# Kernel optimization log

Measured on AMD Instinct MI355X. Metric: run time of the kernel, lower is better.

## Reference

```python
import jax, jax.numpy as jnp
import numpy as np

HEADS = 16
HEAD_DIM = 64
DIM = 1024
WH, WW = 32, 32
ROPE_DIM = 32  # = HEAD_DIM // 2
ROPE_BASE = 10000
EPS = 1e-6


def _rope_cache():
    # theta: [ROPE_DIM//2]
    theta = 1.0 / (ROPE_BASE ** (jnp.arange(0, ROPE_DIM, 2, dtype=jnp.float32)[: ROPE_DIM // 2] / ROPE_DIM))
    n = WH * WW
    idx = jnp.arange(n, dtype=jnp.float32)
    x_pos = idx % WW
    y_pos = idx // WW
    freqs = jnp.concatenate([x_pos[:, None] * theta[None, :], y_pos[:, None] * theta[None, :]], axis=-1)  # [n, ROPE_DIM]
    return jnp.cos(freqs), jnp.sin(freqs)


def _apply_rope(x, cos, sin):
    # x: [b, h, n, HEAD_DIM] -> pairs [b, h, n, ROPE_DIM, 2]
    xf = x.astype(jnp.float32).reshape(*x.shape[:-1], -1, 2)
    x0, x1 = xf[..., 0], xf[..., 1]
    c = cos[None, None, :, :]
    s = sin[None, None, :, :]
    out = jnp.stack([x0 * c - x1 * s, x1 * c + x0 * s], axis=-1)
    return out.reshape(*x.shape).astype(x.dtype)


def setup_inputs() -> dict:
    key = jax.random.key(0)
    ks = jax.random.split(key, 5)
    b, n = 16, WH * WW
    inner = HEADS * HEAD_DIM
    return {
        "x": jax.random.normal(ks[0], (b, n, DIM), dtype=jnp.float32),
        "t": jax.random.normal(ks[1], (b, DIM), dtype=jnp.float32),
        "norm_w": jnp.ones((DIM,), dtype=jnp.float32),
        "mod_w": jax.random.normal(ks[2], (2 * DIM, DIM), dtype=jnp.float32) * (DIM ** -0.5),
        "qkv_w": jax.random.normal(ks[3], (3 * inner, DIM), dtype=jnp.float32) * (DIM ** -0.5),
        "wo_w": jax.random.normal(ks[4], (DIM, inner), dtype=jnp.float32) * (inner ** -0.5),
    }


def reference(x, t, norm_w, mod_w, qkv_w, wo_w):
    b, n, dim = x.shape
    scale = HEAD_DIM ** -0.5

    # Modulated RMSNorm
    xf = x.astype(jnp.float32)
    xn = (xf * jax.lax.rsqrt(jnp.mean(xf * xf, axis=-1, keepdims=True) + EPS)).astype(x.dtype) * norm_w
    mod = t @ mod_w.T  # [b, 2*dim]
    sc, sh = mod[:, :dim], mod[:, dim:]
    h = xn * (1.0 + sc[:, None, :]) + sh[:, None, :]

    # QKV projection; rearrange 'b n (h d) -> b h n d' with d = 3*HEAD_DIM, THEN chunk
    qkv = h @ qkv_w.T  # [b, n, 3*inner]
    qkv = qkv.reshape(b, n, HEADS, 3 * HEAD_DIM).transpose(0, 2, 1, 3)  # [b, H, n, 3*hd]
    q, k, v = qkv[..., :HEAD_DIM], qkv[..., HEAD_DIM:2 * HEAD_DIM], qkv[..., 2 * HEAD_DIM:]

    # 2D axial RoPE on q, k
    cos, sin = _rope_cache()
    q = _apply_rope(q, cos, sin)
    k = _apply_rope(k, cos, sin)

    # SDPA (non-causal)
    attn = jax.nn.softmax(jnp.einsum('bhqd,bhkd->bhqk', q * scale, k), axis=-1)
    out = jnp.einsum('bhqk,bhkd->bhqd', attn, v)  # [b, H, n, hd]
    out = out.transpose(0, 2, 1, 3).reshape(b, n, HEADS * HEAD_DIM)
    return out @ wo_w.T
```

## Files before the change

### kernel.cpp

```cpp
#include <hip/hip_runtime.h>
#include <stdint.h>

typedef __bf16    bf16x8 __attribute__((ext_vector_type(8)));
typedef float     f32x4  __attribute__((ext_vector_type(4)));
typedef _Float16  f16;
typedef _Float16  f16x2  __attribute__((ext_vector_type(2)));
typedef _Float16  f16x4  __attribute__((ext_vector_type(4)));
typedef _Float16  f16x8  __attribute__((ext_vector_type(8)));

#define DEV __device__ __forceinline__

DEV ushort f2bf(float f) {
  union { float f; uint32_t u; } v; v.f = f;
  uint32_t u = v.u;
  return (ushort)((u + 0x7fffu + ((u >> 16) & 1u)) >> 16);
}

DEV f16x2 cvt_pkrtz(float a, float b) {
  return __builtin_bit_cast(f16x2, __builtin_amdgcn_cvt_pkrtz(a, b));
}

DEV void async16(const void* g, void* l) {
  __builtin_amdgcn_global_load_lds(
      (__attribute__((address_space(1))) void*)(uintptr_t)g,
      (__attribute__((address_space(3))) void*)(uint32_t)(uintptr_t)l,
      16, 0, 0);
}

__global__ __launch_bounds__(256)
void prep_kernel(const float* __restrict__ t, const float* __restrict__ mw,
                 float* __restrict__ mod,
                 const float* __restrict__ qkvw, ushort* __restrict__ wqk,
                 ushort* __restrict__ wv,
                 const float* __restrict__ wow, ushort* __restrict__ wowb) {
  const int id = blockIdx.x;
  const int tid = threadIdx.x;
  if (id < 2048) {
    const int j = id;
    const int w = tid >> 6, lane = tid & 63;
    float wr[16];
#pragma unroll
    for (int i = 0; i < 16; ++i) wr[i] = mw[(size_t)j * 1024 + lane + i * 64];
#pragma unroll
    for (int bb = 0; bb < 4; ++bb) {
      int b = w * 4 + bb;
      float s = 0.f;
#pragma unroll
      for (int i = 0; i < 16; ++i) s += wr[i] * t[b * 1024 + lane + i * 64];
#pragma unroll
      for (int m = 32; m >= 1; m >>= 1) s += __shfl_xor(s, m, 64);
      if (lane == 0) mod[b * 2048 + j] = s;
    }
  } else if (id < 5120) {
    const int j = id - 2048;
    uint32_t hd = (uint32_t)j / 192u;
    uint32_t rem = (uint32_t)j - hd * 192u;
    ushort* dst = (rem < 128u) ? (wqk + (size_t)(hd * 128u + rem) * 1024)
                               : (wv + (size_t)(hd * 64u + (rem - 128u)) * 1024);
    float4 v = ((const float4*)(qkvw + (size_t)j * 1024))[tid];
    ushort4 o;
    o.x = f2bf(v.x); o.y = f2bf(v.y); o.z = f2bf(v.z); o.w = f2bf(v.w);
    ((ushort4*)dst)[tid] = o;
  } else {
    const int i = (id - 5120) * 256 + tid;
    float4 v = ((const float4*)wow)[i];
    ushort4 o;
    o.x = f2bf(v.x); o.y = f2bf(v.y); o.z = f2bf(v.z); o.w = f2bf(v.w);
    ((ushort4*)wowb)[i] = o;
  }
}

__global__ __launch_bounds__(256)
void rms_mod_kernel(const float* __restrict__ x, const float* __restrict__ nw,
                    const float* __restrict__ mod, ushort* __restrict__ h) {
  int row = blockIdx.x;
  int b = row >> 10;
  int tid = threadIdx.x;
  const float4 xv = *(const float4*)(x + (size_t)row * 1024 + tid * 4);
  float ss = xv.x * xv.x + xv.y * xv.y + xv.z * xv.z + xv.w * xv.w;
#pragma unroll
  for (int m = 32; m >= 1; m >>= 1) ss += __shfl_xor(ss, m, 64);
  __shared__ float red[4];
  int w = tid >> 6, lane = tid & 63;
  if (lane == 0) red[w] = ss;
  __syncthreads();
  float tot = red[0] + red[1] + red[2] + red[3];
  float rn = rsqrtf(tot * (1.f / 1024.f) + 1e-6f);
  float4 wv = *(const float4*)(nw + tid * 4);
  float4 sc = *(const float4*)(mod + (size_t)b * 2048 + tid * 4);
  float4 sh = *(const float4*)(mod + (size_t)b * 2048 + 1024 + tid * 4);
  ushort4 o;
  o.x = f2bf(xv.x * rn * wv.x * (1.f + sc.x) + sh.x);
  o.y = f2bf(xv.y * rn * wv.y * (1.f + sc.y) + sh.y);
  o.z = f2bf(xv.z * rn * wv.z * (1.f + sc.z) + sh.z);
  o.w = f2bf(xv.w * rn * wv.w * (1.f + sc.w) + sh.w);
  *(ushort4*)(h + (size_t)row * 1024 + tid * 4) = o;
}

__global__ __launch_bounds__(512, 2)
void gemm_qkv_kernel(const ushort* __restrict__ hbuf, const ushort* __restrict__ wqk,
                     const ushort* __restrict__ wvw,
                     f16* __restrict__ qb, f16* __restrict__ kb,
                     f16* __restrict__ vtb) {
  __shared__ ushort smem[65536];
  const int id0 = blockIdx.x;
  const int id = (id0 & 7) * 96 + (id0 >> 3);
  int mode, m0, n0;
  const ushort *A, *B;
  if (id < 512) {
    mode = 1; m0 = (id >> 3) * 256; n0 = (id & 7) * 256; A = hbuf; B = wqk;
  } else {
    const int i2 = id - 512;
    mode = 2; n0 = (i2 >> 2) * 256; m0 = (i2 & 3) * 256; A = wvw; B = hbuf;
  }
  const int tid = threadIdx.x;
  const int w = tid >> 6, lane = tid & 63, quad = lane >> 4, l15 = lane & 15;
  const int wm = w >> 2, wn = w & 3;

  const int srow = tid >> 3;
  const int sch  = (tid & 7) ^ (srow & 7);
  const int soff = srow * 1024 + sch * 8;
  const ushort* const Abase = A + (size_t)m0 * 1024;
  const ushort* const Bbase = B + (size_t)n0 * 1024;
  ushort* const As0 = smem;
  ushort* const Bs0 = smem + 32768;
  const int sdst = tid * 8;

#define STG_A(d, t, h) do { \
    async16(Abase + (h) * 131072 + soff + (t) * 64,          As0 + (d) * 16384 + (h) * 8192 + sdst); \
    async16(Abase + (h) * 131072 + 65536 + soff + (t) * 64,  As0 + (d) * 16384 + (h) * 8192 + 4096 + sdst); } while (0)
#define STG_B(d, t, h) do { \
    async16(Bbase + (h) * 131072 + soff + (t) * 64,          Bs0 + (d) * 16384 + (h) * 8192 + sdst); \
    async16(Bbase + (h) * 131072 + 65536 + soff + (t) * 64,  Bs0 + (d) * 16384 + (h) * 8192 + 4096 + sdst); } while (0)

  int aoff[2], boff[2];
#pragma unroll
  for (int kk = 0; kk < 2; ++kk) {
    const int swz = (((kk * 4 + quad) ^ (l15 & 7)) * 8);
    aoff[kk] = (wm * 128 + l15) * 64 + swz;
    boff[kk] = (wn * 64 + l15) * 64 + swz;
  }

  const f32x4 fzero = {0.f, 0.f, 0.f, 0.f};
  f32x4 acc[8][4];
#pragma unroll
  for (int a = 0; a < 8; ++a)
#pragma unroll
    for (int b = 0; b < 4; ++b) acc[a][b] = fzero;

  STG_A(0, 0, 0); STG_A(0, 0, 1); STG_B(0, 0, 0); STG_B(0, 0, 1);
  asm volatile("s_waitcnt vmcnt(0)" ::: "memory");
  __builtin_amdgcn_s_barrier();

  bf16x8 af[4][2];
  bf16x8 bfp[4][2];
#pragma unroll 2
  for (int t = 0; t < 16; ++t) {
    const int cur = t & 1, nxt = cur ^ 1;
    const int tn = (t < 15) ? t + 1 : 15;
    const ushort* Asc = As0 + cur * 16384;
    const ushort* Bsc = Bs0 + cur * 16384;

    STG_A(nxt, tn, 0); STG_A(nxt, tn, 1);
    STG_B(nxt, tn, 0); STG_B(nxt, tn, 1);
#pragma unroll
    for (int nf = 0; nf < 4; ++nf)
#pragma unroll
      for (int kk = 0; kk < 2; ++kk)
        bfp[nf][kk] = *(const bf16x8*)(Bsc + nf * 1024 + boff[kk]);
#pragma unroll
    for (int mf = 0; mf < 4; ++mf)
#pragma unroll
      for (int kk = 0; kk < 2; ++kk)
        af[mf][kk] = *(const bf16x8*)(Asc + mf * 1024 + aoff[kk]);
    __builtin_amdgcn_s_barrier();
    __builtin_amdgcn_s_setprio(1);
#pragma unroll
    for (int mf = 0; mf < 4; ++mf)
#pragma unroll
      for (int nf = 0; nf < 4; ++nf)
#pragma unroll
        for (int kk = 0; kk < 2; ++kk)
          acc[mf][nf] = __builtin_amdgcn_mfma_f32_16x16x32_bf16(
              af[mf][kk], bfp[nf][kk], acc[mf][nf], 0, 0, 0);
    __builtin_amdgcn_s_setprio(0);
    __builtin_amdgcn_s_barrier();

#pragma unroll
    for (int mf = 0; mf < 4; ++mf)
#pragma unroll
      for (int kk = 0; kk < 2; ++kk)
        af[mf][kk] = *(const bf16x8*)(Asc + (4 + mf) * 1024 + aoff[kk]);
    __builtin_amdgcn_s_barrier();
    __builtin_amdgcn_s_setprio(1);
#pragma unroll
    for (int mf = 0; mf < 4; ++mf)
#pragma unroll
      for (int nf = 0; nf < 4; ++nf)
#pragma unroll
        for (int kk = 0; kk < 2; ++kk)
          acc[4 + mf][nf] = __builtin_amdgcn_mfma_f32_16x16x32_bf16(
              af[mf][kk], bfp[nf][kk], acc[4 + mf][nf], 0, 0, 0);
    __builtin_amdgcn_s_setprio(0);
    asm volatile("s_waitcnt vmcnt(0)" ::: "memory");
    __builtin_amdgcn_s_barrier();
  }
#undef STG_A
#undef STG_B

  ushort* eps = smem + w * 8192;
#pragma unroll
  for (int mf = 0; mf < 8; ++mf)
#pragma unroll
    for (int nf = 0; nf < 4; ++nf)
#pragma unroll
      for (int r = 0; r < 4; ++r) {
        const int row_loc = mf * 16 + quad * 4 + r;
        const int col = nf * 16 + l15;
        const int ch = (col >> 3) ^ (row_loc & 7);
        union { f16 h; ushort u; } cv;
        cv.h = (f16)acc[mf][nf][r];
        eps[row_loc * 64 + ch * 8 + (col & 7)] = cv.u;
      }

  const int ch = lane & 7;
  const int rbase = lane >> 3;
  const int gcol = n0 + wn * 64;
  if (mode == 1) {
    const int hd = gcol >> 7, part = (gcol >> 6) & 1;
    const float QS = part ? 1.f : 0.125f * 1.44269504f;
    f16* const outp = part ? kb : qb;
    float th[4];
#pragma unroll
    for (int t2 = 0; t2 < 4; ++t2)
      th[t2] = __expf(-(float)((ch * 4 + t2) & 15) * 0.5756462732485114f);
#pragma unroll
    for (int i = 0; i < 16; ++i) {
      const int row_loc = i * 8 + rbase;
      union { uint4 u4; f16 h[8]; } uv;
      uv.u4 = *(const uint4*)(eps + row_loc * 64 + ((ch ^ (row_loc & 7)) * 8));
      const int m = m0 + wm * 128 + row_loc;
      const int n = m & 1023;
      const float xpos = (float)(n & 31), ypos = (float)(n >> 5);
#pragma unroll
      for (int t2 = 0; t2 < 4; ++t2) {
        const int p = ch * 4 + t2;
        const float pos = (p < 16) ? xpos : ypos;
        float sn, cs;
        __sincosf(pos * th[t2], &sn, &cs);
        const float x0 = (float)uv.h[2 * t2], x1 = (float)uv.h[2 * t2 + 1];
        f16x2 ro = cvt_pkrtz((x0 * cs - x1 * sn) * QS, (x1 * cs + x0 * sn) * QS);
        uv.h[2 * t2] = ro[0];
        uv.h[2 * t2 + 1] = ro[1];
      }
      f16* dst = outp + (((size_t)((m >> 10) * 16 + hd) * 1024 + n) * 64 + ch * 8);
      *(uint4*)dst = uv.u4;
    }
  } else {
    const int b = gcol >> 10, tb = gcol & 1023;
#pragma unroll
    for (int i = 0; i < 16; ++i) {
      const int row_loc = i * 8 + rbase;
      uint4 v = *(const uint4*)(eps + row_loc * 64 + ((ch ^ (row_loc & 7)) * 8));
      if (i & 1) { unsigned t0 = v.x, t1 = v.y; v.x = v.z; v.y = v.w; v.z = t0; v.w = t1; }
      const int m = m0 + wm * 128 + row_loc;
      f16* dst = vtb + ((size_t)(b * 1024 + m) * 1024 + tb + ch * 8);
      *(uint4*)dst = v;
    }
  }
}

__global__ __launch_bounds__(512, 2)
void gemm_wo_kernel(const ushort* __restrict__ A, const ushort* __restrict__ B,
                    float* __restrict__ outf) {
  __shared__ ushort smem[65536];
  const int id0 = blockIdx.x;
  const int id = (id0 & 7) * 32 + (id0 >> 3);
  const int m0 = (id >> 2) * 256, n0 = (id & 3) * 256;
  const int tid = threadIdx.x;
  const int w = tid >> 6, lane = tid & 63, quad = lane >> 4, l15 = lane & 15;
  const int wm = w >> 2, wn = w & 3;

  const int srow = tid >> 3;
  const int sch  = (tid & 7) ^ (srow & 7);
  const int soff = srow * 1024 + sch * 8;
  const int b0 = m0 >> 10, nb = m0 & 1023;
  const ushort* const Abase = A + (size_t)b0 * 16 * 65536 + (size_t)nb * 64;
  const ushort* const Bbase = B + (size_t)n0 * 1024;
  ushort* const As0 = smem;
  ushort* const Bs0 = smem + 32768;
  const int sdst = tid * 8;

#define STG_A(d, t, h) do { \
    async16(Abase + (size_t)(t) * 65536 + ((h) * 128 + srow) * 64 + sch * 8,      As0 + (d) * 16384 + (h) * 8192 + sdst); \
    async16(Abase + (size_t)(t) * 65536 + ((h) * 128 + 64 + srow) * 64 + sch * 8, As0 + (d) * 16384 + (h) * 8192 + 4096 + sdst); } while (0)
#define STG_B(d, t, h) do { \
    async16(Bbase + (h) * 131072 + soff + (t) * 64,          Bs0 + (d) * 16384 + (h) * 8192 + sdst); \
    async16(Bbase + (h) * 131072 + 65536 + soff + (t) * 64,  Bs0 + (d) * 16384 + (h) * 8192 + 4096 + sdst); } while (0)

  int aoff[2], boff[2];
#pragma unroll
  for (int kk = 0; kk < 2; ++kk) {
    const int swz = (((kk * 4 + quad) ^ (l15 & 7)) * 8);
    aoff[kk] = (wm * 128 + l15) * 64 + swz;
    boff[kk] = (wn * 64 + l15) * 64 + swz;
  }

  const f32x4 fzero = {0.f, 0.f, 0.f, 0.f};
  f32x4 acc[8][4];
#pragma unroll
  for (int a = 0; a < 8; ++a)
#pragma unroll
    for (int b = 0; b < 4; ++b) acc[a][b] = fzero;

  STG_A(0, 0, 0); STG_A(0, 0, 1); STG_B(0, 0, 0); STG_B(0, 0, 1);
  asm volatile("s_waitcnt vmcnt(0)" ::: "memory");
  __builtin_amdgcn_s_barrier();

  bf16x8 af[4][2];
  bf16x8 bfp[4][2];
#pragma unroll 2
  for (int t = 0; t < 16; ++t) {
    const int cur = t & 1, nxt = cur ^ 1;
    const int tn = (t < 15) ? t + 1 : 15;
    const ushort* Asc = As0 + cur * 16384;
    const ushort* Bsc = Bs0 + cur * 16384;

    STG_A(nxt, tn, 0); STG_A(nxt, tn, 1);
    STG_B(nxt, tn, 0); STG_B(nxt, tn, 1);
#pragma unroll
    for (int nf = 0; nf < 4; ++nf)
#pragma unroll
      for (int kk = 0; kk < 2; ++kk)
        bfp[nf][kk] = *(const bf16x8*)(Bsc + nf * 1024 + boff[kk]);
#pragma unroll
    for (int mf = 0; mf < 4; ++mf)
#pragma unroll
      for (int kk = 0; kk < 2; ++kk)
        af[mf][kk] = *(const bf16x8*)(Asc + mf * 1024 + aoff[kk]);
    __builtin_amdgcn_s_barrier();
    __builtin_amdgcn_s_setprio(1);
#pragma unroll
    for (int mf = 0; mf < 4; ++mf)
#pragma unroll
      for (int nf = 0; nf < 4; ++nf)
#pragma unroll
        for (int kk = 0; kk < 2; ++kk)
          acc[mf][nf] = __builtin_amdgcn_mfma_f32_16x16x32_bf16(
              af[mf][kk], bfp[nf][kk], acc[mf][nf], 0, 0, 0);
    __builtin_amdgcn_s_setprio(0);
    __builtin_amdgcn_s_barrier();

#pragma unroll
    for (int mf = 0; mf < 4; ++mf)
#pragma unroll
      for (int kk = 0; kk < 2; ++kk)
        af[mf][kk] = *(const bf16x8*)(Asc + (4 + mf) * 1024 + aoff[kk]);
    __builtin_amdgcn_s_barrier();
    __builtin_amdgcn_s_setprio(1);
#pragma unroll
    for (int mf = 0; mf < 4; ++mf)
#pragma unroll
      for (int nf = 0; nf < 4; ++nf)
#pragma unroll
        for (int kk = 0; kk < 2; ++kk)
          acc[4 + mf][nf] = __builtin_amdgcn_mfma_f32_16x16x32_bf16(
              af[mf][kk], bfp[nf][kk], acc[4 + mf][nf], 0, 0, 0);
    __builtin_amdgcn_s_setprio(0);
    asm volatile("s_waitcnt vmcnt(0)" ::: "memory");
    __builtin_amdgcn_s_barrier();
  }
#undef STG_A
#undef STG_B

#pragma unroll
  for (int mf = 0; mf < 8; ++mf)
#pragma unroll
    for (int nf = 0; nf < 4; ++nf) {
      const int col = n0 + wn * 64 + nf * 16 + l15;
#pragma unroll
      for (int r = 0; r < 4; ++r) {
        const int row = m0 + wm * 128 + mf * 16 + quad * 4 + r;
        outf[(size_t)row * 1024 + col] = acc[mf][nf][r];
      }
    }
}

__global__ __launch_bounds__(256, 2)
void attn_kernel(const f16* __restrict__ qbuf, const f16* __restrict__ kbuf,
                 const f16* __restrict__ vtbuf, ushort* __restrict__ aout) {
  __shared__ f16 Ks[2][128 * 64];
  __shared__ f16 Vs[2][64 * 128];

  const int id = blockIdx.x;
  const int xcd = id & 7, j = id >> 3;
  const int bh = xcd * 32 + (j >> 3);
  const int q0 = (j & 7) * 128;
  const f16* Qg = qbuf + (size_t)bh * 1024 * 64;
  const f16* Kg = kbuf + (size_t)bh * 1024 * 64;
  const f16* Vg = vtbuf + (size_t)bh * 64 * 1024;
  const int tid = threadIdx.x;
  const int w = tid >> 6, lane = tid & 63, quad = lane >> 4, l15 = lane & 15;
  const f32x4 fzero = {0.f, 0.f, 0.f, 0.f};

  f16x8 qf[2][2];
#pragma unroll
  for (int qs = 0; qs < 2; ++qs)
#pragma unroll
    for (int dc = 0; dc < 2; ++dc)
      qf[qs][dc] = *(const f16x8*)(Qg + (size_t)(q0 + w * 32 + qs * 16 + l15) * 64 +
                                   dc * 32 + quad * 8);

  f32x4 oacc[2][4];
#pragma unroll
  for (int qs = 0; qs < 2; ++qs)
#pragma unroll
    for (int ds = 0; ds < 4; ++ds) oacc[qs][ds] = fzero;
  float mrun[2] = {-1e30f, -1e30f}, lrun[2] = {0.f, 0.f};

#pragma unroll
  for (int i = 0; i < 4; ++i) {
    int u = i * 256 + tid, r = u >> 3, c = u & 7;
    async16(Kg + (size_t)r * 64 + (c ^ (r & 7)) * 8, &Ks[0][u * 8]);
  }
#pragma unroll
  for (int i = 0; i < 4; ++i) {
    int u = i * 256 + tid, r = u >> 4, c = u & 15;
    async16(Vg + (size_t)r * 1024 + (c ^ (r & 15)) * 8, &Vs[0][u * 8]);
  }
  __syncthreads();

#pragma unroll 2
  for (int kt = 0; kt < 1024; kt += 128) {
    const int cur = (kt >> 7) & 1;
    if (kt + 128 < 1024) {
      const int nkt = kt + 128;
#pragma unroll
      for (int i = 0; i < 4; ++i) {
        int u = i * 256 + tid, r = u >> 3, c = u & 7;
        async16(Kg + (size_t)(nkt + r) * 64 + (c ^ (r & 7)) * 8, &Ks[cur ^ 1][u * 8]);
      }
#pragma unroll
      for (int i = 0; i < 4; ++i) {
        int u = i * 256 + tid, r = u >> 4, c = u & 15;
        async16(Vg + (size_t)r * 1024 + nkt + (c ^ (r & 15)) * 8, &Vs[cur ^ 1][u * 8]);
      }
    }
    const f16* Ksc = Ks[cur];
    const f16* Vsc = Vs[cur];

    f32x4 sacc[2][8];
#pragma unroll
    for (int qs = 0; qs < 2; ++qs)
#pragma unroll
      for (int ks = 0; ks < 8; ++ks) sacc[qs][ks] = fzero;
#pragma unroll
    for (int ks = 0; ks < 8; ++ks) {
#pragma unroll
      for (int dc = 0; dc < 2; ++dc) {
        int row = ks * 16 + l15;
        int ch = (dc * 4 + quad) ^ (row & 7);
        f16x8 kf = *(const f16x8*)(Ksc + row * 64 + ch * 8);
        sacc[0][ks] = __builtin_amdgcn_mfma_f32_16x16x32_f16(kf, qf[0][dc], sacc[0][ks], 0, 0, 0);
        sacc[1][ks] = __builtin_amdgcn_mfma_f32_16x16x32_f16(kf, qf[1][dc], sacc[1][ks], 0, 0, 0);
      }
    }

    f16x4 pf[2][8];
#pragma unroll
    for (int qs = 0; qs < 2; ++qs) {
      const float* sv = (const float*)&sacc[qs][0];
      float mx = fmaxf(sv[0], sv[1]);
#pragma unroll
      for (int k = 2; k < 32; k += 2)
        mx = fmaxf(fmaxf(mx, sv[k]), sv[k + 1]);
      mx = fmaxf(mx, __shfl_xor(mx, 16, 64));
      mx = fmaxf(mx, __shfl_xor(mx, 32, 64));
      if (__any(mx - mrun[qs] > 8.f)) {
        float mnew = fmaxf(mrun[qs], mx);
        float alpha = __builtin_amdgcn_exp2f(mrun[qs] - mnew);
        mrun[qs] = mnew;
        lrun[qs] *= alpha;
        float ar[4];
#pragma unroll
        for (int r = 0; r < 4; ++r) ar[r] = __shfl(alpha, quad * 4 + r, 64);
#pragma unroll
        for (int ds = 0; ds < 4; ++ds)
#pragma unroll
          for (int r = 0; r < 4; ++r) oacc[qs][ds][r] *= ar[r];
      }
      const float mnew = mrun[qs];
      float rs = 0.f;
#pragma unroll
      for (int ks = 0; ks < 8; ++ks) {
        float p0 = __builtin_amdgcn_exp2f(sacc[qs][ks][0] - mnew);
        float p1 = __builtin_amdgcn_exp2f(sacc[qs][ks][1] - mnew);
        float p2 = __builtin_amdgcn_exp2f(sacc[qs][ks][2] - mnew);
        float p3 = __builtin_amdgcn_exp2f(sacc[qs][ks][3] - mnew);
        rs += (p0 + p1) + (p2 + p3);
        union { f16x4 v; f16x2 h[2]; } pu;
        pu.h[0] = cvt_pkrtz(p0, p1);
        pu.h[1] = cvt_pkrtz(p2, p3);
        pf[qs][ks] = pu.v;
      }
      rs += __shfl_xor(rs, 16, 64);
      rs += __shfl_xor(rs, 32, 64);
      lrun[qs] += rs;
    }

#pragma unroll
    for (int ks = 0; ks < 8; ++ks) {
#pragma unroll
      for (int ds = 0; ds < 4; ++ds) {
        int row = ds * 16 + l15;
        int c16 = ks * 2 + (quad >> 1);
        int half = (quad & 1) ^ ((l15 >> 3) & 1);
        f16x4 vf = *(const f16x4*)(Vsc + row * 128 + ((c16 ^ (row & 15)) * 8) + half * 4);
        oacc[0][ds] = __builtin_amdgcn_mfma_f32_16x16x16f16(pf[0][ks], vf, oacc[0][ds], 0, 0, 0);
        oacc[1][ds] = __builtin_amdgcn_mfma_f32_16x16x16f16(pf[1][ks], vf, oacc[1][ds], 0, 0, 0);
      }
    }
    __syncthreads();
  }

  ushort* eps = (ushort*)&Ks[0][0] + w * 2048;
#pragma unroll
  for (int qs = 0; qs < 2; ++qs) {
    float linv[4];
#pragma unroll
    for (int r = 0; r < 4; ++r)
      linv[r] = __builtin_amdgcn_rcpf(__shfl(lrun[qs], quad * 4 + r, 64));
#pragma unroll
    for (int ds = 0; ds < 4; ++ds)
#pragma unroll
      for (int r = 0; r < 4; ++r) {
        int row_loc = qs * 16 + quad * 4 + r;
        int col = ds * 16 + l15;
        int ch = (col >> 3) ^ (row_loc & 7);
        eps[row_loc * 64 + ch * 8 + (col & 7)] = f2bf(oacc[qs][ds][r] * linv[r]);
      }
  }
  __syncthreads();
  const size_t obase = ((size_t)bh * 1024 + q0 + w * 32) * 64;
#pragma unroll
  for (int i = 0; i < 4; ++i) {
    int row_loc = i * 8 + (lane >> 3);
    int ch = lane & 7;
    uint4 v = *(const uint4*)(eps + row_loc * 64 + ((ch ^ (row_loc & 7)) * 8));
    *(uint4*)(aout + obase + row_loc * 64 + ch * 8) = v;
  }
}

extern "C" void kernel_launch(void* const* d_in, const int* in_sizes, int n_in,
                              void* d_out, int out_size, void* d_ws, size_t ws_size,
                              hipStream_t stream) {
  const float* x    = (const float*)d_in[0];
  const float* t    = (const float*)d_in[1];
  const float* nw   = (const float*)d_in[2];
  const float* mw   = (const float*)d_in[3];
  const float* qkvw = (const float*)d_in[4];
  const float* wow  = (const float*)d_in[5];
  float* out = (float*)d_out;
  char* ws = (char*)d_ws;

  float*  modbuf  = (float*)(ws);
  ushort* hbuf    = (ushort*)(ws + 131072);
  ushort* wqk_b   = (ushort*)(ws + 33685504);
  ushort* wv_b    = (ushort*)(ws + 37879808);
  ushort* wow_b   = (ushort*)(ws + 39976960);
  f16*    qbuf    = (f16*)(ws + 42074112);
  f16*    kbuf    = (f16*)(ws + 75628544);
  f16*    vtbuf   = (f16*)(ws + 109182976);
  ushort* abuf    = (ushort*)(ws + 142737408);

  prep_kernel<<<dim3(6144), dim3(256), 0, stream>>>(
      t, mw, modbuf, qkvw, wqk_b, wv_b, wow, wow_b);
  rms_mod_kernel<<<dim3(16384), dim3(256), 0, stream>>>(x, nw, modbuf, hbuf);
  gemm_qkv_kernel<<<dim3(768), dim3(512), 0, stream>>>(
      hbuf, wqk_b, wv_b, qbuf, kbuf, vtbuf);
  attn_kernel<<<dim3(2048), dim3(256), 0, stream>>>(qbuf, kbuf, vtbuf, abuf);
  gemm_wo_kernel<<<dim3(256), dim3(512), 0, stream>>>(abuf, wow_b, out);
}
```

Measured before the change: 391.4 us.

## Restage QKV GEMM into finer-grained ping-pong and shrink attention KV tiles

```diff
diff --git a/kernel.cpp b/kernel.cpp
--- a/kernel.cpp
+++ b/kernel.cpp
@@ -97,6 +97,37 @@
   *(ushort4*)(h + (size_t)row * 1024 + tid * 4) = o;
 }
 
+DEV void lda2(bf16x8 (&af)[4][2], const ushort* base, const int (&aoff)[2]) {
+#pragma unroll
+  for (int mf = 0; mf < 4; ++mf)
+#pragma unroll
+    for (int kk = 0; kk < 2; ++kk)
+      af[mf][kk] = *(const bf16x8*)(base + mf * 1024 + aoff[kk]);
+}
+DEV void ldb2(bf16x8 (&bf)[2][2], const ushort* base, const int (&boff)[2]) {
+#pragma unroll
+  for (int nf = 0; nf < 2; ++nf)
+#pragma unroll
+    for (int kk = 0; kk < 2; ++kk)
+      bf[nf][kk] = *(const bf16x8*)(base + nf * 1024 + boff[kk]);
+}
+template <int MH, int NH>
+DEV void mm16(f32x4 (&acc)[8][4], const bf16x8 (&af)[4][2], const bf16x8 (&bf)[2][2]) {
+#pragma unroll
+  for (int mf = 0; mf < 4; ++mf)
+#pragma unroll
+    for (int nf = 0; nf < 2; ++nf)
+#pragma unroll
+      for (int kk = 0; kk < 2; ++kk)
+        acc[MH * 4 + mf][NH * 2 + nf] = __builtin_amdgcn_mfma_f32_16x16x32_bf16(
+            af[mf][kk], bf[nf][kk], acc[MH * 4 + mf][NH * 2 + nf], 0, 0, 0);
+}
+#define BARR __builtin_amdgcn_s_barrier()
+#define PRIO1 __builtin_amdgcn_s_setprio(1)
+#define PRIO0 __builtin_amdgcn_s_setprio(0)
+#define VMC4 asm volatile("s_waitcnt vmcnt(4)" ::: "memory")
+#define VMC0 asm volatile("s_waitcnt vmcnt(0)" ::: "memory")
+
 __global__ __launch_bounds__(512, 2)
 void gemm_qkv_kernel(const ushort* __restrict__ hbuf, const ushort* __restrict__ wqk,
                      const ushort* __restrict__ wvw,
@@ -148,63 +179,61 @@
 #pragma unroll
     for (int b = 0; b < 4; ++b) acc[a][b] = fzero;
 
+  bf16x8 af[4][2];
+  bf16x8 bfA[2][2];
+  bf16x8 bfB[2][2];
+
   STG_A(0, 0, 0); STG_A(0, 0, 1); STG_B(0, 0, 0); STG_B(0, 0, 1);
-  asm volatile("s_waitcnt vmcnt(0)" ::: "memory");
-  __builtin_amdgcn_s_barrier();
-
-  bf16x8 af[4][2];
-  bf16x8 bfp[4][2];
-#pragma unroll 2
-  for (int t = 0; t < 16; ++t) {
-    const int cur = t & 1, nxt = cur ^ 1;
-    const int tn = (t < 15) ? t + 1 : 15;
-    const ushort* Asc = As0 + cur * 16384;
-    const ushort* Bsc = Bs0 + cur * 16384;
-
-    STG_A(nxt, tn, 0); STG_A(nxt, tn, 1);
-    STG_B(nxt, tn, 0); STG_B(nxt, tn, 1);
-#pragma unroll
-    for (int nf = 0; nf < 4; ++nf)
-#pragma unroll
-      for (int kk = 0; kk < 2; ++kk)
-        bfp[nf][kk] = *(const bf16x8*)(Bsc + nf * 1024 + boff[kk]);
-#pragma unroll
-    for (int mf = 0; mf < 4; ++mf)
-#pragma unroll
-      for (int kk = 0; kk < 2; ++kk)
-        af[mf][kk] = *(const bf16x8*)(Asc + mf * 1024 + aoff[kk]);
-    __builtin_amdgcn_s_barrier();
-    __builtin_amdgcn_s_setprio(1);
-#pragma unroll
-    for (int mf = 0; mf < 4; ++mf)
-#pragma unroll
-      for (int nf = 0; nf < 4; ++nf)
-#pragma unroll
-        for (int kk = 0; kk < 2; ++kk)
-          acc[mf][nf] = __builtin_amdgcn_mfma_f32_16x16x32_bf16(
-              af[mf][kk], bfp[nf][kk], acc[mf][nf], 0, 0, 0);
-    __builtin_amdgcn_s_setprio(0);
-    __builtin_amdgcn_s_barrier();
-
-#pragma unroll
-    for (int mf = 0; mf < 4; ++mf)
-#pragma unroll
-      for (int kk = 0; kk < 2; ++kk)
-        af[mf][kk] = *(const bf16x8*)(Asc + (4 + mf) * 1024 + aoff[kk]);
-    __builtin_amdgcn_s_barrier();
-    __builtin_amdgcn_s_setprio(1);
-#pragma unroll
-    for (int mf = 0; mf < 4; ++mf)
-#pragma unroll
-      for (int nf = 0; nf < 4; ++nf)
-#pragma unroll
-        for (int kk = 0; kk < 2; ++kk)
-          acc[4 + mf][nf] = __builtin_amdgcn_mfma_f32_16x16x32_bf16(
-              af[mf][kk], bfp[nf][kk], acc[4 + mf][nf], 0, 0, 0);
-    __builtin_amdgcn_s_setprio(0);
-    asm volatile("s_waitcnt vmcnt(0)" ::: "memory");
-    __builtin_amdgcn_s_barrier();
-  }
+  STG_A(1, 1, 0); STG_A(1, 1, 1);
+  VMC4;
+  BARR;
+
+#pragma unroll 1
+  for (int i = 0; i < 7; ++i) {
+    const int t1 = 2 * i + 1, u0 = 2 * i + 2, u1 = 2 * i + 3;
+    lda2(af, As0, aoff);
+    ldb2(bfA, Bs0, boff);
+    STG_B(1, t1, 0); STG_B(1, t1, 1);
+    BARR; PRIO1; mm16<0, 0>(acc, af, bfA); PRIO0; BARR;
+    ldb2(bfB, Bs0 + 2048, boff);
+    BARR; PRIO1; mm16<0, 1>(acc, af, bfB); PRIO0; BARR;
+    lda2(af, As0 + 4096, aoff);
+    BARR; PRIO1; mm16<1, 1>(acc, af, bfB); PRIO0; BARR;
+    ldb2(bfA, Bs0, boff);
+    STG_A(0, u0, 0); STG_A(0, u0, 1);
+    BARR; PRIO1; mm16<1, 0>(acc, af, bfA); PRIO0;
+    VMC4; BARR;
+    lda2(af, As0 + 16384, aoff);
+    ldb2(bfA, Bs0 + 16384, boff);
+    STG_B(0, u0, 0); STG_B(0, u0, 1);
+    BARR; PRIO1; mm16<0, 0>(acc, af, bfA); PRIO0; BARR;
+    ldb2(bfB, Bs0 + 16384 + 2048, boff);
+    BARR; PRIO1; mm16<0, 1>(acc, af, bfB); PRIO0; BARR;
+    lda2(af, As0 + 16384 + 4096, aoff);
+    BARR; PRIO1; mm16<1, 1>(acc, af, bfB); PRIO0; BARR;
+    ldb2(bfA, Bs0 + 16384, boff);
+    STG_A(1, u1, 0); STG_A(1, u1, 1);
+    BARR; PRIO1; mm16<1, 0>(acc, af, bfA); PRIO0;
+    VMC4; BARR;
+  }
+  lda2(af, As0, aoff); ldb2(bfA, Bs0, boff);
+  STG_B(1, 15, 0); STG_B(1, 15, 1);
+  BARR; PRIO1; mm16<0, 0>(acc, af, bfA); PRIO0; BARR;
+  ldb2(bfB, Bs0 + 2048, boff);
+  BARR; PRIO1; mm16<0, 1>(acc, af, bfB); PRIO0; BARR;
+  lda2(af, As0 + 4096, aoff);
+  BARR; PRIO1; mm16<1, 1>(acc, af, bfB); PRIO0; BARR;
+  ldb2(bfA, Bs0, boff);
+  BARR; PRIO1; mm16<1, 0>(acc, af, bfA); PRIO0;
+  VMC0; BARR;
+  lda2(af, As0 + 16384, aoff); ldb2(bfA, Bs0 + 16384, boff);
+  BARR; PRIO1; mm16<0, 0>(acc, af, bfA); PRIO0; BARR;
+  ldb2(bfB, Bs0 + 16384 + 2048, boff);
+  BARR; PRIO1; mm16<0, 1>(acc, af, bfB); PRIO0; BARR;
+  lda2(af, As0 + 16384 + 4096, aoff);
+  BARR; PRIO1; mm16<1, 1>(acc, af, bfB); PRIO0; BARR;
+  ldb2(bfA, Bs0 + 16384, boff);
+  BARR; PRIO1; mm16<1, 0>(acc, af, bfA); PRIO0; BARR;
 #undef STG_A
 #undef STG_B
 
@@ -313,12 +342,12 @@
 #pragma unroll
     for (int b = 0; b < 4; ++b) acc[a][b] = fzero;
 
-  STG_A(0, 0, 0); STG_A(0, 0, 1); STG_B(0, 0, 0); STG_B(0, 0, 1);
-  asm volatile("s_waitcnt vmcnt(0)" ::: "memory");
-  __builtin_amdgcn_s_barrier();
-
   bf16x8 af[4][2];
   bf16x8 bfp[4][2];
+  STG_A(0, 0, 0); STG_A(0, 0, 1); STG_B(0, 0, 0); STG_B(0, 0, 1);
+  VMC0;
+  BARR;
+
 #pragma unroll 2
   for (int t = 0; t < 16; ++t) {
     const int cur = t & 1, nxt = cur ^ 1;
@@ -338,8 +367,7 @@
 #pragma unroll
       for (int kk = 0; kk < 2; ++kk)
         af[mf][kk] = *(const bf16x8*)(Asc + mf * 1024 + aoff[kk]);
-    __builtin_amdgcn_s_barrier();
-    __builtin_amdgcn_s_setprio(1);
+    BARR; PRIO1;
 #pragma unroll
     for (int mf = 0; mf < 4; ++mf)
 #pragma unroll
@@ -348,16 +376,14 @@
         for (int kk = 0; kk < 2; ++kk)
           acc[mf][nf] = __builtin_amdgcn_mfma_f32_16x16x32_bf16(
               af[mf][kk], bfp[nf][kk], acc[mf][nf], 0, 0, 0);
-    __builtin_amdgcn_s_setprio(0);
-    __builtin_amdgcn_s_barrier();
+    PRIO0; BARR;
 
 #pragma unroll
     for (int mf = 0; mf < 4; ++mf)
 #pragma unroll
       for (int kk = 0; kk < 2; ++kk)
         af[mf][kk] = *(const bf16x8*)(Asc + (4 + mf) * 1024 + aoff[kk]);
-    __builtin_amdgcn_s_barrier();
-    __builtin_amdgcn_s_setprio(1);
+    BARR; PRIO1;
 #pragma unroll
     for (int mf = 0; mf < 4; ++mf)
 #pragma unroll
@@ -366,9 +392,9 @@
         for (int kk = 0; kk < 2; ++kk)
           acc[4 + mf][nf] = __builtin_amdgcn_mfma_f32_16x16x32_bf16(
               af[mf][kk], bfp[nf][kk], acc[4 + mf][nf], 0, 0, 0);
-    __builtin_amdgcn_s_setprio(0);
-    asm volatile("s_waitcnt vmcnt(0)" ::: "memory");
-    __builtin_amdgcn_s_barrier();
+    PRIO0;
+    VMC0;
+    BARR;
   }
 #undef STG_A
 #undef STG_B
@@ -386,11 +412,11 @@
     }
 }
 
-__global__ __launch_bounds__(256, 2)
+__global__ __launch_bounds__(256, 4)
 void attn_kernel(const f16* __restrict__ qbuf, const f16* __restrict__ kbuf,
                  const f16* __restrict__ vtbuf, ushort* __restrict__ aout) {
-  __shared__ f16 Ks[2][128 * 64];
-  __shared__ f16 Vs[2][64 * 128];
+  __shared__ f16 Ks[2][64 * 64];
+  __shared__ f16 Vs[2][64 * 64];
 
   const int id = blockIdx.x;
   const int xcd = id & 7, j = id >> 3;
@@ -419,43 +445,43 @@
   float mrun[2] = {-1e30f, -1e30f}, lrun[2] = {0.f, 0.f};
 
 #pragma unroll
-  for (int i = 0; i < 4; ++i) {
+  for (int i = 0; i < 2; ++i) {
     int u = i * 256 + tid, r = u >> 3, c = u & 7;
     async16(Kg + (size_t)r * 64 + (c ^ (r & 7)) * 8, &Ks[0][u * 8]);
   }
 #pragma unroll
-  for (int i = 0; i < 4; ++i) {
-    int u = i * 256 + tid, r = u >> 4, c = u & 15;
-    async16(Vg + (size_t)r * 1024 + (c ^ (r & 15)) * 8, &Vs[0][u * 8]);
+  for (int i = 0; i < 2; ++i) {
+    int u = i * 256 + tid, r = u >> 3, c = u & 7;
+    async16(Vg + (size_t)r * 1024 + (c ^ (r & 7)) * 8, &Vs[0][u * 8]);
   }
   __syncthreads();
 
 #pragma unroll 2
-  for (int kt = 0; kt < 1024; kt += 128) {
-    const int cur = (kt >> 7) & 1;
-    if (kt + 128 < 1024) {
-      const int nkt = kt + 128;
-#pragma unroll
-      for (int i = 0; i < 4; ++i) {
+  for (int kt = 0; kt < 1024; kt += 64) {
+    const int cur = (kt >> 6) & 1;
+    if (kt + 64 < 1024) {
+      const int nkt = kt + 64;
+#pragma unroll
+      for (int i = 0; i < 2; ++i) {
         int u = i * 256 + tid, r = u >> 3, c = u & 7;
         async16(Kg + (size_t)(nkt + r) * 64 + (c ^ (r & 7)) * 8, &Ks[cur ^ 1][u * 8]);
       }
 #pragma unroll
-      for (int i = 0; i < 4; ++i) {
-        int u = i * 256 + tid, r = u >> 4, c = u & 15;
-        async16(Vg + (size_t)r * 1024 + nkt + (c ^ (r & 15)) * 8, &Vs[cur ^ 1][u * 8]);
+      for (int i = 0; i < 2; ++i) {
+        int u = i * 256 + tid, r = u >> 3, c = u & 7;
+        async16(Vg + (size_t)r * 1024 + nkt + (c ^ (r & 7)) * 8, &Vs[cur ^ 1][u * 8]);
       }
     }
     const f16* Ksc = Ks[cur];
     const f16* Vsc = Vs[cur];
 
-    f32x4 sacc[2][8];
+    f32x4 sacc[2][4];
 #pragma unroll
     for (int qs = 0; qs < 2; ++qs)
 #pragma unroll
-      for (int ks = 0; ks < 8; ++ks) sacc[qs][ks] = fzero;
-#pragma unroll
-    for (int ks = 0; ks < 8; ++ks) {
+      for (int ks = 0; ks < 4; ++ks) sacc[qs][ks] = fzero;
+#pragma unroll
+    for (int ks = 0; ks < 4; ++ks) {
 #pragma unroll
       for (int dc = 0; dc < 2; ++dc) {
         int row = ks * 16 + l15;
@@ -466,13 +492,13 @@
       }
     }
 
-    f16x4 pf[2][8];
+    f16x4 pf[2][4];
 #pragma unroll
     for (int qs = 0; qs < 2; ++qs) {
       const float* sv = (const float*)&sacc[qs][0];
       float mx = fmaxf(sv[0], sv[1]);
 #pragma unroll
-      for (int k = 2; k < 32; k += 2)
+      for (int k = 2; k < 16; k += 2)
         mx = fmaxf(fmaxf(mx, sv[k]), sv[k + 1]);
       mx = fmaxf(mx, __shfl_xor(mx, 16, 64));
       mx = fmaxf(mx, __shfl_xor(mx, 32, 64));
@@ -492,7 +518,7 @@
       const float mnew = mrun[qs];
       float rs = 0.f;
 #pragma unroll
-      for (int ks = 0; ks < 8; ++ks) {
+      for (int ks = 0; ks < 4; ++ks) {
         float p0 = __builtin_amdgcn_exp2f(sacc[qs][ks][0] - mnew);
         float p1 = __builtin_amdgcn_exp2f(sacc[qs][ks][1] - mnew);
         float p2 = __builtin_amdgcn_exp2f(sacc[qs][ks][2] - mnew);
@@ -509,13 +535,13 @@
     }
 
 #pragma unroll
-    for (int ks = 0; ks < 8; ++ks) {
+    for (int ks = 0; ks < 4; ++ks) {
 #pragma unroll
       for (int ds = 0; ds < 4; ++ds) {
         int row = ds * 16 + l15;
         int c16 = ks * 2 + (quad >> 1);
         int half = (quad & 1) ^ ((l15 >> 3) & 1);
-        f16x4 vf = *(const f16x4*)(Vsc + row * 128 + ((c16 ^ (row & 15)) * 8) + half * 4);
+        f16x4 vf = *(const f16x4*)(Vsc + row * 64 + ((c16 ^ (row & 7)) * 8) + half * 4);
         oacc[0][ds] = __builtin_amdgcn_mfma_f32_16x16x16f16(pf[0][ks], vf, oacc[0][ds], 0, 0, 0);
         oacc[1][ds] = __builtin_amdgcn_mfma_f32_16x16x16f16(pf[1][ks], vf, oacc[1][ds], 0, 0, 0);
       }
```

After: 384.7 us. About the same (-1.7%).

## Shrink attention KV tile to raise occupancy and drop GEMM intra-loop barriers

Applied to the files above, without the earlier changes.

```diff
diff --git a/kernel.cpp b/kernel.cpp
--- a/kernel.cpp
+++ b/kernel.cpp
@@ -97,6 +97,16 @@
   *(ushort4*)(h + (size_t)row * 1024 + tid * 4) = o;
 }
 
+DEV void lda2(bf16x8 (&af)[4][2], const ushort* base, const int (&aoff)[2]) {
+#pragma unroll
+  for (int mf = 0; mf < 4; ++mf)
+#pragma unroll
+    for (int kk = 0; kk < 2; ++kk)
+      af[mf][kk] = *(const bf16x8*)(base + mf * 1024 + aoff[kk]);
+}
+#define PRIO1 __builtin_amdgcn_s_setprio(1)
+#define PRIO0 __builtin_amdgcn_s_setprio(0)
+
 __global__ __launch_bounds__(512, 2)
 void gemm_qkv_kernel(const ushort* __restrict__ hbuf, const ushort* __restrict__ wqk,
                      const ushort* __restrict__ wvw,
@@ -148,12 +158,12 @@
 #pragma unroll
     for (int b = 0; b < 4; ++b) acc[a][b] = fzero;
 
-  STG_A(0, 0, 0); STG_A(0, 0, 1); STG_B(0, 0, 0); STG_B(0, 0, 1);
-  asm volatile("s_waitcnt vmcnt(0)" ::: "memory");
-  __builtin_amdgcn_s_barrier();
-
   bf16x8 af[4][2];
   bf16x8 bfp[4][2];
+
+  STG_A(0, 0, 0); STG_A(0, 0, 1); STG_B(0, 0, 0); STG_B(0, 0, 1);
+  __syncthreads();
+
 #pragma unroll 2
   for (int t = 0; t < 16; ++t) {
     const int cur = t & 1, nxt = cur ^ 1;
@@ -163,18 +173,14 @@
 
     STG_A(nxt, tn, 0); STG_A(nxt, tn, 1);
     STG_B(nxt, tn, 0); STG_B(nxt, tn, 1);
+
 #pragma unroll
     for (int nf = 0; nf < 4; ++nf)
 #pragma unroll
       for (int kk = 0; kk < 2; ++kk)
         bfp[nf][kk] = *(const bf16x8*)(Bsc + nf * 1024 + boff[kk]);
-#pragma unroll
-    for (int mf = 0; mf < 4; ++mf)
-#pragma unroll
-      for (int kk = 0; kk < 2; ++kk)
-        af[mf][kk] = *(const bf16x8*)(Asc + mf * 1024 + aoff[kk]);
-    __builtin_amdgcn_s_barrier();
-    __builtin_amdgcn_s_setprio(1);
+    lda2(af, Asc, aoff);
+    PRIO1;
 #pragma unroll
     for (int mf = 0; mf < 4; ++mf)
 #pragma unroll
@@ -183,16 +189,9 @@
         for (int kk = 0; kk < 2; ++kk)
           acc[mf][nf] = __builtin_amdgcn_mfma_f32_16x16x32_bf16(
               af[mf][kk], bfp[nf][kk], acc[mf][nf], 0, 0, 0);
-    __builtin_amdgcn_s_setprio(0);
-    __builtin_amdgcn_s_barrier();
-
-#pragma unroll
-    for (int mf = 0; mf < 4; ++mf)
-#pragma unroll
-      for (int kk = 0; kk < 2; ++kk)
-        af[mf][kk] = *(const bf16x8*)(Asc + (4 + mf) * 1024 + aoff[kk]);
-    __builtin_amdgcn_s_barrier();
-    __builtin_amdgcn_s_setprio(1);
+    PRIO0;
+    lda2(af, Asc + 4096, aoff);
+    PRIO1;
 #pragma unroll
     for (int mf = 0; mf < 4; ++mf)
 #pragma unroll
@@ -201,9 +200,8 @@
         for (int kk = 0; kk < 2; ++kk)
           acc[4 + mf][nf] = __builtin_amdgcn_mfma_f32_16x16x32_bf16(
               af[mf][kk], bfp[nf][kk], acc[4 + mf][nf], 0, 0, 0);
-    __builtin_amdgcn_s_setprio(0);
-    asm volatile("s_waitcnt vmcnt(0)" ::: "memory");
-    __builtin_amdgcn_s_barrier();
+    PRIO0;
+    __syncthreads();
   }
 #undef STG_A
 #undef STG_B
@@ -313,12 +311,11 @@
 #pragma unroll
     for (int b = 0; b < 4; ++b) acc[a][b] = fzero;
 
-  STG_A(0, 0, 0); STG_A(0, 0, 1); STG_B(0, 0, 0); STG_B(0, 0, 1);
-  asm volatile("s_waitcnt vmcnt(0)" ::: "memory");
-  __builtin_amdgcn_s_barrier();
-
   bf16x8 af[4][2];
   bf16x8 bfp[4][2];
+  STG_A(0, 0, 0); STG_A(0, 0, 1); STG_B(0, 0, 0); STG_B(0, 0, 1);
+  __syncthreads();
+
 #pragma unroll 2
   for (int t = 0; t < 16; ++t) {
     const int cur = t & 1, nxt = cur ^ 1;
@@ -333,13 +330,8 @@
 #pragma unroll
       for (int kk = 0; kk < 2; ++kk)
         bfp[nf][kk] = *(const bf16x8*)(Bsc + nf * 1024 + boff[kk]);
-#pragma unroll
-    for (int mf = 0; mf < 4; ++mf)
-#pragma unroll
-      for (int kk = 0; kk < 2; ++kk)
-        af[mf][kk] = *(const bf16x8*)(Asc + mf * 1024 + aoff[kk]);
-    __builtin_amdgcn_s_barrier();
-    __builtin_amdgcn_s_setprio(1);
+    lda2(af, Asc, aoff);
+    PRIO1;
 #pragma unroll
     for (int mf = 0; mf < 4; ++mf)
 #pragma unroll
@@ -348,16 +340,9 @@
         for (int kk = 0; kk < 2; ++kk)
           acc[mf][nf] = __builtin_amdgcn_mfma_f32_16x16x32_bf16(
               af[mf][kk], bfp[nf][kk], acc[mf][nf], 0, 0, 0);
-    __builtin_amdgcn_s_setprio(0);
-    __builtin_amdgcn_s_barrier();
-
-#pragma unroll
-    for (int mf = 0; mf < 4; ++mf)
-#pragma unroll
-      for (int kk = 0; kk < 2; ++kk)
-        af[mf][kk] = *(const bf16x8*)(Asc + (4 + mf) * 1024 + aoff[kk]);
-    __builtin_amdgcn_s_barrier();
-    __builtin_amdgcn_s_setprio(1);
+    PRIO0;
+    lda2(af, Asc + 4096, aoff);
+    PRIO1;
 #pragma unroll
     for (int mf = 0; mf < 4; ++mf)
 #pragma unroll
@@ -366,9 +351,8 @@
         for (int kk = 0; kk < 2; ++kk)
           acc[4 + mf][nf] = __builtin_amdgcn_mfma_f32_16x16x32_bf16(
               af[mf][kk], bfp[nf][kk], acc[4 + mf][nf], 0, 0, 0);
-    __builtin_amdgcn_s_setprio(0);
-    asm volatile("s_waitcnt vmcnt(0)" ::: "memory");
-    __builtin_amdgcn_s_barrier();
+    PRIO0;
+    __syncthreads();
   }
 #undef STG_A
 #undef STG_B
@@ -386,11 +370,11 @@
     }
 }
 
-__global__ __launch_bounds__(256, 2)
+__global__ __launch_bounds__(256, 4)
 void attn_kernel(const f16* __restrict__ qbuf, const f16* __restrict__ kbuf,
                  const f16* __restrict__ vtbuf, ushort* __restrict__ aout) {
-  __shared__ f16 Ks[2][128 * 64];
-  __shared__ f16 Vs[2][64 * 128];
+  __shared__ f16 Ks[2][64 * 64];
+  __shared__ f16 Vs[2][64 * 64];
 
   const int id = blockIdx.x;
   const int xcd = id & 7, j = id >> 3;
@@ -419,43 +403,43 @@
   float mrun[2] = {-1e30f, -1e30f}, lrun[2] = {0.f, 0.f};
 
 #pragma unroll
-  for (int i = 0; i < 4; ++i) {
+  for (int i = 0; i < 2; ++i) {
     int u = i * 256 + tid, r = u >> 3, c = u & 7;
     async16(Kg + (size_t)r * 64 + (c ^ (r & 7)) * 8, &Ks[0][u * 8]);
   }
 #pragma unroll
-  for (int i = 0; i < 4; ++i) {
-    int u = i * 256 + tid, r = u >> 4, c = u & 15;
-    async16(Vg + (size_t)r * 1024 + (c ^ (r & 15)) * 8, &Vs[0][u * 8]);
+  for (int i = 0; i < 2; ++i) {
+    int u = i * 256 + tid, r = u >> 3, c = u & 7;
+    async16(Vg + (size_t)r * 1024 + (c ^ (r & 7)) * 8, &Vs[0][u * 8]);
   }
   __syncthreads();
 
 #pragma unroll 2
-  for (int kt = 0; kt < 1024; kt += 128) {
-    const int cur = (kt >> 7) & 1;
-    if (kt + 128 < 1024) {
-      const int nkt = kt + 128;
-#pragma unroll
-      for (int i = 0; i < 4; ++i) {
+  for (int kt = 0; kt < 1024; kt += 64) {
+    const int cur = (kt >> 6) & 1;
+    if (kt + 64 < 1024) {
+      const int nkt = kt + 64;
+#pragma unroll
+      for (int i = 0; i < 2; ++i) {
         int u = i * 256 + tid, r = u >> 3, c = u & 7;
         async16(Kg + (size_t)(nkt + r) * 64 + (c ^ (r & 7)) * 8, &Ks[cur ^ 1][u * 8]);
       }
 #pragma unroll
-      for (int i = 0; i < 4; ++i) {
-        int u = i * 256 + tid, r = u >> 4, c = u & 15;
-        async16(Vg + (size_t)r * 1024 + nkt + (c ^ (r & 15)) * 8, &Vs[cur ^ 1][u * 8]);
+      for (int i = 0; i < 2; ++i) {
+        int u = i * 256 + tid, r = u >> 3, c = u & 7;
+        async16(Vg + (size_t)r * 1024 + nkt + (c ^ (r & 7)) * 8, &Vs[cur ^ 1][u * 8]);
       }
     }
     const f16* Ksc = Ks[cur];
     const f16* Vsc = Vs[cur];
 
-    f32x4 sacc[2][8];
+    f32x4 sacc[2][4];
 #pragma unroll
     for (int qs = 0; qs < 2; ++qs)
 #pragma unroll
-      for (int ks = 0; ks < 8; ++ks) sacc[qs][ks] = fzero;
-#pragma unroll
-    for (int ks = 0; ks < 8; ++ks) {
+      for (int ks = 0; ks < 4; ++ks) sacc[qs][ks] = fzero;
+#pragma unroll
+    for (int ks = 0; ks < 4; ++ks) {
 #pragma unroll
       for (int dc = 0; dc < 2; ++dc) {
         int row = ks * 16 + l15;
@@ -466,13 +450,13 @@
       }
     }
 
-    f16x4 pf[2][8];
+    f16x4 pf[2][4];
 #pragma unroll
     for (int qs = 0; qs < 2; ++qs) {
       const float* sv = (const float*)&sacc[qs][0];
       float mx = fmaxf(sv[0], sv[1]);
 #pragma unroll
-      for (int k = 2; k < 32; k += 2)
+      for (int k = 2; k < 16; k += 2)
         mx = fmaxf(fmaxf(mx, sv[k]), sv[k + 1]);
       mx = fmaxf(mx, __shfl_xor(mx, 16, 64));
       mx = fmaxf(mx, __shfl_xor(mx, 32, 64));
@@ -492,7 +476,7 @@
       const float mnew = mrun[qs];
       float rs = 0.f;
 #pragma unroll
-      for (int ks = 0; ks < 8; ++ks) {
+      for (int ks = 0; ks < 4; ++ks) {
         float p0 = __builtin_amdgcn_exp2f(sacc[qs][ks][0] - mnew);
         float p1 = __builtin_amdgcn_exp2f(sacc[qs][ks][1] - mnew);
         float p2 = __builtin_amdgcn_exp2f(sacc[qs][ks][2] - mnew);
@@ -509,13 +493,13 @@
     }
 
 #pragma unroll
-    for (int ks = 0; ks < 8; ++ks) {
+    for (int ks = 0; ks < 4; ++ks) {
 #pragma unroll
       for (int ds = 0; ds < 4; ++ds) {
         int row = ds * 16 + l15;
         int c16 = ks * 2 + (quad >> 1);
         int half = (quad & 1) ^ ((l15 >> 3) & 1);
-        f16x4 vf = *(const f16x4*)(Vsc + row * 128 + ((c16 ^ (row & 15)) * 8) + half * 4);
+        f16x4 vf = *(const f16x4*)(Vsc + row * 64 + ((c16 ^ (row & 7)) * 8) + half * 4);
         oacc[0][ds] = __builtin_amdgcn_mfma_f32_16x16x16f16(pf[0][ks], vf, oacc[0][ds], 0, 0, 0);
         oacc[1][ds] = __builtin_amdgcn_mfma_f32_16x16x16f16(pf[1][ks], vf, oacc[1][ds], 0, 0, 0);
       }
```

Measured after the change: 384.3 us. No clear change (-1.8%).
